# Performance work log

Hardware: AMD Instinct MI355X
Metric: run time of the kernel (lower is better)

## Reference

```python
import jax, jax.numpy as jnp
import numpy as np

N, E, DIN, HID, DOUT = 50000, 800000, 128, 128, 64
NEG_SLOPE = 0.2


def setup_inputs() -> dict:
    key = jax.random.key(0)
    ks = jax.random.split(key, 16)
    x = jax.random.normal(ks[0], (N, DIN), dtype=jnp.float32)
    edge_index = jax.random.randint(ks[1], (2, E), 0, N, dtype=jnp.int64)

    def lin(k, fan_in, fan_out):
        kw, kb = jax.random.split(k)
        s = 1.0 / np.sqrt(fan_in)
        W = jax.random.uniform(kw, (fan_in, fan_out), jnp.float32, -s, s)
        b = jax.random.uniform(kb, (fan_out,), jnp.float32, -s, s)
        return W, b

    Wl, bl = lin(ks[2], DIN, DIN)   # GATv2 lin_l
    Wr, br = lin(ks[3], DIN, DIN)   # GATv2 lin_r
    att = jax.random.uniform(ks[4], (DIN,), jnp.float32, -1.0 / np.sqrt(DIN), 1.0 / np.sqrt(DIN))
    bg = jnp.zeros((DIN,), jnp.float32)  # GAT output bias
    W1, b1 = lin(ks[5], DIN, HID)   # ChebConv K=1 -> plain linear
    W2, b2 = lin(ks[6], HID, HID)
    W3, b3 = lin(ks[7], HID, DOUT)
    return {"x": x, "edge_index": edge_index, "Wl": Wl, "bl": bl, "Wr": Wr,
            "br": br, "att": att, "bg": bg, "W1": W1, "b1": b1,
            "W2": W2, "b2": b2, "W3": W3, "b3": b3}


def reference(x, edge_index, Wl, bl, Wr, br, att, bg, W1, b1, W2, b2, W3, b3):
    n = x.shape[0]
    # GATv2Conv adds self loops by default
    loop = jnp.arange(n, dtype=edge_index.dtype)
    src = jnp.concatenate([edge_index[0], loop])  # source j
    dst = jnp.concatenate([edge_index[1], loop])  # target i

    xl = x @ Wl + bl  # [N, DIN]
    xr = x @ Wr + br  # [N, DIN]

    # GATv2 edge scores: leaky_relu(x_l[j] + x_r[i]) . att
    e = jax.nn.leaky_relu(xl[src] + xr[dst], NEG_SLOPE)  # [E+N, DIN]
    a = e @ att                                          # [E+N]

    # softmax over incoming edges of each destination node
    amax = jax.ops.segment_max(a, dst, num_segments=n)
    ea = jnp.exp(a - amax[dst])
    denom = jax.ops.segment_sum(ea, dst, num_segments=n)
    alpha = ea / denom[dst]                              # [E+N]

    # aggregate messages alpha * x_l[j] at destinations
    h = jax.ops.segment_sum(alpha[:, None] * xl[src], dst, num_segments=n) + bg

    # ChebConv with K=1 reduces to a linear layer (T_0(L) = I)
    h = jax.nn.relu(h @ W1 + b1)
    h = jax.nn.relu(h @ W2 + b2)
    # dropout_rate = 0.0 -> identity
    return h @ W3 + b3
```

## Files before the change

### kernel.cpp

```cpp
#include <hip/hip_runtime.h>
#include <hip/hip_bf16.h>

#define DIN 128
#define NEG_SLOPE 0.2f
#define PTILE 1024
#define CVT_BLKS 289

typedef __attribute__((ext_vector_type(8))) short bf16x8;
typedef __attribute__((ext_vector_type(8))) unsigned short u16x8;
typedef __attribute__((ext_vector_type(4))) float f32x4;
typedef __attribute__((ext_vector_type(2))) float f32x2;
typedef __attribute__((ext_vector_type(4))) unsigned int u32x4;

__device__ __forceinline__ ushort f2bf(float f) {
  unsigned u = __float_as_uint(f);
  u += 0x7FFFu + ((u >> 16) & 1u);
  return (ushort)(u >> 16);
}
__device__ __forceinline__ f32x2 bfpair(unsigned u) {
  f32x2 r;
  r.x = __uint_as_float(u << 16);
  r.y = __uint_as_float(u & 0xFFFF0000u);
  return r;
}

template <int CTRL>
__device__ __forceinline__ float dppadd(float x) {
  int v = __builtin_amdgcn_update_dpp(0, __float_as_int(x), CTRL, 0xf, 0xf, true);
  return x + __int_as_float(v);
}
__device__ __forceinline__ float red16(float t) {
  t = dppadd<0xB1>(t);
  t = dppadd<0x4E>(t);
  t = dppadd<0x141>(t);
  t = dppadd<0x140>(t);
  return t;
}

__global__ __launch_bounds__(256) void cvt_hist_kernel(
    const float* __restrict__ Wl, const float* __restrict__ Wr,
    const float* __restrict__ W1, const float* __restrict__ W2,
    const float* __restrict__ W3,
    ushort* __restrict__ WlT, ushort* __restrict__ WrT,
    ushort* __restrict__ W1T, ushort* __restrict__ W2T,
    ushort* __restrict__ W3T,
    const int* __restrict__ ei, int* __restrict__ ghist,
    int* __restrict__ nhist, int E) {
  if (blockIdx.x < CVT_BLKS) {
    int i = blockIdx.x * 256 + threadIdx.x;
    if (i < 16384) {
      int k = i >> 7, c = i & 127; WlT[c * 128 + k] = f2bf(Wl[i]);
    } else if (i < 32768) {
      int j = i - 16384; int k = j >> 7, c = j & 127; WrT[c * 128 + k] = f2bf(Wr[j]);
    } else if (i < 49152) {
      int j = i - 32768; int k = j >> 7, c = j & 127; W1T[c * 128 + k] = f2bf(W1[j]);
    } else if (i < 65536) {
      int j = i - 49152; int k = j >> 7, c = j & 127; W2T[c * 128 + k] = f2bf(W2[j]);
    } else if (i < 73728) {
      int j = i - 65536; int k = j >> 6, c = j & 63; W3T[c * 128 + k] = f2bf(W3[j]);
    }
  } else {
    __shared__ int h[256];
    h[threadIdx.x] = 0;
    __syncthreads();
    int tile = blockIdx.x - CVT_BLKS;
    for (int e = tile * PTILE + threadIdx.x;
         e < min(E, (tile + 1) * PTILE); e += 256) {
      int d = ei[E + e];
      atomicAdd(&h[d >> 8], 1);
      atomicAdd(&nhist[d], 1);
    }
    __syncthreads();
    if (h[threadIdx.x] > 0) atomicAdd(&ghist[threadIdx.x], h[threadIdx.x]);
  }
}

__global__ __launch_bounds__(256) void lin_partition_kernel(
    const float* __restrict__ x,
    const ushort* __restrict__ WlT, const float* __restrict__ bl,
    const ushort* __restrict__ WrT, const float* __restrict__ br,
    ushort* __restrict__ xl, ushort* __restrict__ xr, int n, int nblk_lin,
    const int* __restrict__ ei, unsigned* __restrict__ part,
    const int* __restrict__ ghist, int* __restrict__ cursor0, int E) {
  if ((int)blockIdx.x < nblk_lin) {
    const int tid = threadIdx.x;
    const int wv = tid >> 6, lane = tid & 63;
    const int m = lane & 15, quad = lane >> 4;
    const int colbase = (wv & 1) * 64;
    const int nodew = blockIdx.x * 32 + (wv >> 1) * 16;
    int arow = nodew + m; if (arow >= n) arow = n - 1;
    f32x4 accl[4], accr[4];
#pragma unroll
    for (int nt = 0; nt < 4; nt++) { accl[nt] = (f32x4){0,0,0,0}; accr[nt] = (f32x4){0,0,0,0}; }
#pragma unroll
    for (int kk = 0; kk < 4; kk++) {
      int k0 = kk * 32 + quad * 8;
      const float4* xp = (const float4*)(x + (long)arow * 128 + k0);
      float4 x0 = xp[0], x1 = xp[1];
      bf16x8 af;
      af[0] = (short)f2bf(x0.x); af[1] = (short)f2bf(x0.y);
      af[2] = (short)f2bf(x0.z); af[3] = (short)f2bf(x0.w);
      af[4] = (short)f2bf(x1.x); af[5] = (short)f2bf(x1.y);
      af[6] = (short)f2bf(x1.z); af[7] = (short)f2bf(x1.w);
#pragma unroll
      for (int nt = 0; nt < 4; nt++) {
        int brow = colbase + nt * 16 + m;
        bf16x8 bl8 = *(const bf16x8*)(WlT + brow * 128 + k0);
        bf16x8 br8 = *(const bf16x8*)(WrT + brow * 128 + k0);
        accl[nt] = __builtin_amdgcn_mfma_f32_16x16x32_bf16(af, bl8, accl[nt], 0, 0, 0);
        accr[nt] = __builtin_amdgcn_mfma_f32_16x16x32_bf16(af, br8, accr[nt], 0, 0, 0);
      }
    }
#pragma unroll
    for (int nt = 0; nt < 4; nt++) {
      int col = colbase + nt * 16 + m;
      float vbl = bl[col], vbr = br[col];
#pragma unroll
      for (int r = 0; r < 4; r++) {
        int node = nodew + quad * 4 + r;
        if (node < n) {
          xl[(long)node * 128 + col] = f2bf(accl[nt][r] + vbl);
          xr[(long)node * 128 + col] = f2bf(accr[nt][r] + vbr);
        }
      }
    }
  } else {
    __shared__ int hist[256], pref[256], sexcl[256], curs[256], gbase[256],
                   gsc[256];
    const int tid = threadIdx.x;
    const int gv0 = ghist[tid];
    gsc[tid] = gv0;
    hist[tid] = 0;
    __syncthreads();
    __shared__ unsigned buf[PTILE];
    const int tile0 = ((int)blockIdx.x - nblk_lin) * PTILE;
    const int tcount = min(PTILE, E - tile0);
    unsigned pk[PTILE / 256];
    int cnt = 0;
    for (int i = tid; i < tcount; i += 256) {
      int e = tile0 + i;
      int s = ei[e], d = ei[E + e];
      unsigned p = ((unsigned)d << 16) | (unsigned)s;
      pk[cnt++] = p;
      atomicAdd(&hist[d >> 8], 1);
    }
    __syncthreads();
    int v = hist[tid];
    pref[tid] = v;
    __syncthreads();
    for (int d = 1; d < 256; d <<= 1) {
      int t1 = (tid >= d) ? pref[tid - d] : 0;
      int t2 = (tid >= d) ? gsc[tid - d] : 0;
      __syncthreads();
      pref[tid] += t1;
      gsc[tid] += t2;
      __syncthreads();
    }
    int exc = pref[tid] - v;
    sexcl[tid] = exc;
    curs[tid] = exc;
    gbase[tid] = (gsc[tid] - gv0) + ((v > 0) ? atomicAdd(&cursor0[tid], v) : 0);
    __syncthreads();
    for (int j = 0; j < cnt; j++) {
      int b = pk[j] >> 24;
      int pos = atomicAdd(&curs[b], 1);
      buf[pos] = pk[j];
    }
    __syncthreads();
    for (int i = tid; i < tcount; i += 256) {
      unsigned p = buf[i];
      int b = p >> 24;
      part[gbase[b] + (i - sexcl[b])] = p;
    }
  }
}

__global__ __launch_bounds__(512) void fine_kernel(
    const unsigned* __restrict__ part, const int* __restrict__ ghist,
    const int* __restrict__ nhist,
    int* __restrict__ offsets, ushort* __restrict__ ssrc,
    int N, int E, int nbuck) {
  __shared__ int gsc[256], nsc[256], curs[256];
  const int tid = threadIdx.x;
  const int b = blockIdx.x;
  int nv = 0;
  if (tid < 256) {
    gsc[tid] = ghist[tid];
    int node = b * 256 + tid;
    nv = (node < N) ? nhist[node] : 0;
    nsc[tid] = nv;
  }
  __syncthreads();
  for (int d = 1; d < 256; d <<= 1) {
    int t1 = (tid >= d && tid < 256) ? gsc[tid - d] : 0;
    int t2 = (tid >= d && tid < 256) ? nsc[tid - d] : 0;
    __syncthreads();
    if (tid < 256) { gsc[tid] += t1; nsc[tid] += t2; }
    __syncthreads();
  }
  const int seg0 = (b == 0) ? 0 : gsc[b - 1];
  const int len = gsc[b] - seg0;
  if (tid < 256) {
    int o = seg0 + nsc[tid] - nv;
    curs[tid] = o;
    int node = b * 256 + tid;
    if (node < N) offsets[node] = o;
  }
  if (b == nbuck - 1 && tid == 0) offsets[N] = E;
  __syncthreads();
  for (int i = tid; i < len; i += 512) {
    unsigned p = part[seg0 + i];
    int pos = atomicAdd(&curs[(p >> 16) & 255], 1);
    ssrc[pos] = (ushort)(p & 0xFFFFu);
  }
}

__global__ __launch_bounds__(256) void node_aggr_kernel(
    const ushort* __restrict__ xl, const ushort* __restrict__ xr,
    const float* __restrict__ att, const float* __restrict__ bg,
    const int* __restrict__ offsets, const ushort* __restrict__ ssrc,
    ushort* __restrict__ h, int n) {
  int wave = (int)((blockIdx.x * (long)blockDim.x + threadIdx.x) >> 6);
  int lane = threadIdx.x & 63;
  if (wave >= n) return;
  const int node = wave;
  const int eg = lane >> 4, sl = lane & 15;
  const int beg = offsets[node];
  const int end = offsets[node + 1];
  const int last = end - 1;
  const ushort* __restrict__ xls = xl + sl * 8;
  int ia0 = beg + 2 * eg;
  int sa  = (int)ssrc[min(ia0, last)];
  int sb  = (int)ssrc[min(ia0 + 1, last)];
  int sa2 = (int)ssrc[min(ia0 + 8, last)];
  int sb2 = (int)ssrc[min(ia0 + 9, last)];
  u32x4 uva = *(const u32x4*)(xls + (long)sa * 128);
  u32x4 uvb = *(const u32x4*)(xls + (long)sb * 128);

  f32x2 a06[4], a04[4], r2[4], acc2[4];
  {
    const float4* ap = (const float4*)(att + sl * 8);
    float4 a0 = ap[0], a1 = ap[1];
    f32x2 av[4] = {{a0.x, a0.y}, {a0.z, a0.w}, {a1.x, a1.y}, {a1.z, a1.w}};
#pragma unroll
    for (int jp = 0; jp < 4; jp++) {
      a06[jp] = 0.6f * av[jp];
      a04[jp] = 0.4f * av[jp];
    }
  }
  u32x4 rv = *(const u32x4*)(xr + (long)node * 128 + sl * 8);
  u32x4 lv = *(const u32x4*)(xls + (long)node * 128);
  float denom;
  {
    f32x2 t1 = {0.f, 0.f}, t2 = {0.f, 0.f};
    f32x2 l2[4];
#pragma unroll
    for (int jp = 0; jp < 4; jp++) {
      r2[jp] = bfpair(rv[jp]);
      l2[jp] = bfpair(lv[jp]);
      f32x2 v = l2[jp] + r2[jp];
      t1 += a06[jp] * v;
      t2 += a04[jp] * __builtin_elementwise_abs(v);
    }
    float t = red16(t1.x + t1.y + t2.x + t2.y);
    float es = __expf(t);
    denom = (eg == 0) ? es : 0.f;
#pragma unroll
    for (int jp = 0; jp < 4; jp++)
      acc2[jp] = (eg == 0) ? es * l2[jp] : (f32x2){0.f, 0.f};
  }
  for (int p = beg; p < end; p += 8) {
    u32x4 ca = uva, cb = uvb;
    int ia = p + 2 * eg;
    bool cva = ia < end, cvb = ia + 1 < end;
    uva = *(const u32x4*)(xls + (long)sa2 * 128);
    uvb = *(const u32x4*)(xls + (long)sb2 * 128);
    int ian = p + 16 + 2 * eg;
    sa2 = (int)ssrc[min(ian, last)];
    sb2 = (int)ssrc[min(ian + 1, last)];
    f32x2 ua2[4], ub2[4];
    f32x2 ta1 = {0.f, 0.f}, ta2 = {0.f, 0.f};
    f32x2 tb1 = {0.f, 0.f}, tb2 = {0.f, 0.f};
#pragma unroll
    for (int jp = 0; jp < 4; jp++) {
      ua2[jp] = bfpair(ca[jp]);
      ub2[jp] = bfpair(cb[jp]);
      f32x2 va2 = ua2[jp] + r2[jp];
      f32x2 vb2 = ub2[jp] + r2[jp];
      ta1 += a06[jp] * va2;
      ta2 += a04[jp] * __builtin_elementwise_abs(va2);
      tb1 += a06[jp] * vb2;
      tb2 += a04[jp] * __builtin_elementwise_abs(vb2);
    }
    float ta = red16(ta1.x + ta1.y + ta2.x + ta2.y);
    float tb = red16(tb1.x + tb1.y + tb2.x + tb2.y);
    float ea = cva ? __expf(ta) : 0.f;
    float eb = cvb ? __expf(tb) : 0.f;
    denom += ea + eb;
#pragma unroll
    for (int jp = 0; jp < 4; jp++)
      acc2[jp] += ea * ua2[jp] + eb * ub2[jp];
  }
#pragma unroll
  for (int jp = 0; jp < 4; jp++) {
    acc2[jp].x += __shfl_xor(acc2[jp].x, 16);
    acc2[jp].y += __shfl_xor(acc2[jp].y, 16);
    acc2[jp].x += __shfl_xor(acc2[jp].x, 32);
    acc2[jp].y += __shfl_xor(acc2[jp].y, 32);
  }
  denom += __shfl_xor(denom, 16);
  denom += __shfl_xor(denom, 32);
  if (eg == 0) {
    float inv = 1.0f / denom;
    const float4* bp = (const float4*)(bg + sl * 8);
    float4 g0 = bp[0], g1 = bp[1];
    f32x2 gv[4] = {{g0.x, g0.y}, {g0.z, g0.w}, {g1.x, g1.y}, {g1.z, g1.w}};
    u16x8 o;
#pragma unroll
    for (int jp = 0; jp < 4; jp++) {
      f32x2 hv = acc2[jp] * inv + gv[jp];
      o[2 * jp]     = f2bf(hv.x);
      o[2 * jp + 1] = f2bf(hv.y);
    }
    *(u16x8*)(h + (long)node * 128 + sl * 8) = o;
  }
}

#define LDSP 136
__global__ __launch_bounds__(256) void mlp_mfma_kernel(
    const ushort* __restrict__ hb,
    const ushort* __restrict__ W1T, const float* __restrict__ b1,
    const ushort* __restrict__ W2T, const float* __restrict__ b2,
    const ushort* __restrict__ W3T, const float* __restrict__ b3,
    float* __restrict__ out, int n) {
  __shared__ ushort act[32][LDSP];
  const int tid = threadIdx.x;
  const int wv = tid >> 6, lane = tid & 63;
  const int m = lane & 15, quad = lane >> 4;
  const int half = wv & 1, ng = wv >> 1;
  const int colbase = half * 64;
  const int nodew = blockIdx.x * 32 + ng * 16;
  int arow = nodew + m; if (arow >= n) arow = n - 1;
  f32x4 acc[4];
#pragma unroll
  for (int nt = 0; nt < 4; nt++) acc[nt] = (f32x4){0,0,0,0};
#pragma unroll
  for (int kk = 0; kk < 4; kk++) {
    int k0 = kk * 32 + quad * 8;
    bf16x8 af = *(const bf16x8*)(hb + (long)arow * 128 + k0);
#pragma unroll
    for (int nt = 0; nt < 4; nt++) {
      bf16x8 b8 = *(const bf16x8*)(W1T + (colbase + nt * 16 + m) * 128 + k0);
      acc[nt] = __builtin_amdgcn_mfma_f32_16x16x32_bf16(af, b8, acc[nt], 0, 0, 0);
    }
  }
#pragma unroll
  for (int nt = 0; nt < 4; nt++) {
    int col = colbase + nt * 16 + m;
    float b = b1[col];
#pragma unroll
    for (int r = 0; r < 4; r++)
      act[ng * 16 + quad * 4 + r][col] = f2bf(fmaxf(acc[nt][r] + b, 0.f));
  }
  __syncthreads();
#pragma unroll
  for (int nt = 0; nt < 4; nt++) acc[nt] = (f32x4){0,0,0,0};
#pragma unroll
  for (int kk = 0; kk < 4; kk++) {
    int k0 = kk * 32 + quad * 8;
    bf16x8 af = *(const bf16x8*)(&act[ng * 16 + m][k0]);
#pragma unroll
    for (int nt = 0; nt < 4; nt++) {
      bf16x8 b8 = *(const bf16x8*)(W2T + (colbase + nt * 16 + m) * 128 + k0);
      acc[nt] = __builtin_amdgcn_mfma_f32_16x16x32_bf16(af, b8, acc[nt], 0, 0, 0);
    }
  }
  __syncthreads();
#pragma unroll
  for (int nt = 0; nt < 4; nt++) {
    int col = colbase + nt * 16 + m;
    float b = b2[col];
#pragma unroll
    for (int r = 0; r < 4; r++)
      act[ng * 16 + quad * 4 + r][col] = f2bf(fmaxf(acc[nt][r] + b, 0.f));
  }
  __syncthreads();
  f32x4 acc3[2];
#pragma unroll
  for (int nt = 0; nt < 2; nt++) acc3[nt] = (f32x4){0,0,0,0};
#pragma unroll
  for (int kk = 0; kk < 4; kk++) {
    int k0 = kk * 32 + quad * 8;
    bf16x8 af = *(const bf16x8*)(&act[ng * 16 + m][k0]);
#pragma unroll
    for (int nt = 0; nt < 2; nt++) {
      bf16x8 b8 = *(const bf16x8*)(W3T + (half * 32 + nt * 16 + m) * 128 + k0);
      acc3[nt] = __builtin_amdgcn_mfma_f32_16x16x32_bf16(af, b8, acc3[nt], 0, 0, 0);
    }
  }
#pragma unroll
  for (int nt = 0; nt < 2; nt++) {
    int col = half * 32 + nt * 16 + m;
    float b = b3[col];
#pragma unroll
    for (int r = 0; r < 4; r++) {
      int node = nodew + quad * 4 + r;
      if (node < n) out[(long)node * 64 + col] = acc3[nt][r] + b;
    }
  }
}

extern "C" void kernel_launch(void* const* d_in, const int* in_sizes, int n_in,
                              void* d_out, int out_size, void* d_ws, size_t ws_size,
                              hipStream_t stream) {
  const float* x   = (const float*)d_in[0];
  const int*   ei  = (const int*)d_in[1];
  const float* Wl  = (const float*)d_in[2];
  const float* bl  = (const float*)d_in[3];
  const float* Wr  = (const float*)d_in[4];
  const float* br  = (const float*)d_in[5];
  const float* att = (const float*)d_in[6];
  const float* bg  = (const float*)d_in[7];
  const float* W1  = (const float*)d_in[8];
  const float* b1  = (const float*)d_in[9];
  const float* W2  = (const float*)d_in[10];
  const float* b2  = (const float*)d_in[11];
  const float* W3  = (const float*)d_in[12];
  const float* b3  = (const float*)d_in[13];
  float* out = (float*)d_out;

  const int N = in_sizes[0] / DIN;
  const int E = in_sizes[1] / 2;
  const int nbuck = (N + 255) >> 8;

  char* ws = (char*)d_ws;
  size_t off = 0;
  auto alloc = [&](size_t bytes) {
    void* p = ws + off;
    off += (bytes + 255) & ~(size_t)255;
    return p;
  };
  int* ghist     = (int*)alloc(256 * 4);
  int* cursor0   = (int*)alloc(256 * 4);
  int* nhist     = (int*)alloc((size_t)N * 4);
  int* offsets   = (int*)alloc(((size_t)N + 4) * 4);
  unsigned* part = (unsigned*)alloc((size_t)E * 4);
  ushort* ssrc   = (ushort*)alloc(((size_t)E + 16) * 2);
  ushort* xlb    = (ushort*)alloc((size_t)N * DIN * 2);
  ushort* xrb    = (ushort*)alloc((size_t)N * DIN * 2);
  ushort* hbf    = (ushort*)alloc((size_t)N * DIN * 2);
  ushort* WlT    = (ushort*)alloc(16384 * 2);
  ushort* WrT    = (ushort*)alloc(16384 * 2);
  ushort* W1T    = (ushort*)alloc(16384 * 2);
  ushort* W2T    = (ushort*)alloc(16384 * 2);
  ushort* W3T    = (ushort*)alloc(8192 * 2);
  (void)ws_size;

  hipMemsetAsync(ghist, 0, 2048 + (size_t)N * 4, stream);

  int ntile = (E + PTILE - 1) / PTILE;
  cvt_hist_kernel<<<CVT_BLKS + ntile, 256, 0, stream>>>(
      Wl, Wr, W1, W2, W3, WlT, WrT, W1T, W2T, W3T, ei, ghist, nhist, E);

  int nblk32 = (N + 31) / 32;
  lin_partition_kernel<<<nblk32 + ntile, 256, 0, stream>>>(
      x, WlT, bl, WrT, br, xlb, xrb, N, nblk32, ei, part, ghist, cursor0, E);

  fine_kernel<<<nbuck, 512, 0, stream>>>(part, ghist, nhist, offsets, ssrc,
                                         N, E, nbuck);

  int nwblk = (N + 3) / 4;
  node_aggr_kernel<<<nwblk, 256, 0, stream>>>(xlb, xrb, att, bg,
                                              offsets, ssrc, hbf, N);

  mlp_mfma_kernel<<<nblk32, 256, 0, stream>>>(hbf, W1T, b1, W2T, b2,
                                              W3T, b3, out, N);
}
```

Baseline: 281.5 us.

## Compute per-node degree counts in fine kernel LDS instead of global atomics

```diff
diff --git a/kernel.cpp b/kernel.cpp
--- a/kernel.cpp
+++ b/kernel.cpp
@@ -3,7 +3,8 @@
 
 #define DIN 128
 #define NEG_SLOPE 0.2f
-#define PTILE 1024
+#define PTILE 2048
+#define FCAP 8192
 #define CVT_BLKS 289
 
 typedef __attribute__((ext_vector_type(8))) short bf16x8;
@@ -44,8 +45,7 @@
     ushort* __restrict__ WlT, ushort* __restrict__ WrT,
     ushort* __restrict__ W1T, ushort* __restrict__ W2T,
     ushort* __restrict__ W3T,
-    const int* __restrict__ ei, int* __restrict__ ghist,
-    int* __restrict__ nhist, int E) {
+    const int* __restrict__ ei, int* __restrict__ ghist, int E) {
   if (blockIdx.x < CVT_BLKS) {
     int i = blockIdx.x * 256 + threadIdx.x;
     if (i < 16384) {
@@ -65,11 +65,8 @@
     __syncthreads();
     int tile = blockIdx.x - CVT_BLKS;
     for (int e = tile * PTILE + threadIdx.x;
-         e < min(E, (tile + 1) * PTILE); e += 256) {
-      int d = ei[E + e];
-      atomicAdd(&h[d >> 8], 1);
-      atomicAdd(&nhist[d], 1);
-    }
+         e < min(E, (tile + 1) * PTILE); e += 256)
+      atomicAdd(&h[ei[E + e] >> 8], 1);
     __syncthreads();
     if (h[threadIdx.x] > 0) atomicAdd(&ghist[threadIdx.x], h[threadIdx.x]);
   }
@@ -175,41 +172,52 @@
   }
 }
 
-__global__ __launch_bounds__(512) void fine_kernel(
+__global__ __launch_bounds__(1024) void fine_kernel(
     const unsigned* __restrict__ part, const int* __restrict__ ghist,
-    const int* __restrict__ nhist,
     int* __restrict__ offsets, ushort* __restrict__ ssrc,
     int N, int E, int nbuck) {
-  __shared__ int gsc[256], nsc[256], curs[256];
+  __shared__ int hist[256], gsc[256], curs[256];
+  __shared__ unsigned buf[FCAP];
   const int tid = threadIdx.x;
   const int b = blockIdx.x;
-  int nv = 0;
   if (tid < 256) {
     gsc[tid] = ghist[tid];
-    int node = b * 256 + tid;
-    nv = (node < N) ? nhist[node] : 0;
-    nsc[tid] = nv;
+    hist[tid] = 0;
   }
   __syncthreads();
   for (int d = 1; d < 256; d <<= 1) {
-    int t1 = (tid >= d && tid < 256) ? gsc[tid - d] : 0;
-    int t2 = (tid >= d && tid < 256) ? nsc[tid - d] : 0;
-    __syncthreads();
-    if (tid < 256) { gsc[tid] += t1; nsc[tid] += t2; }
+    int t = (tid >= d && tid < 256) ? gsc[tid - d] : 0;
+    __syncthreads();
+    if (tid < 256) gsc[tid] += t;
     __syncthreads();
   }
   const int seg0 = (b == 0) ? 0 : gsc[b - 1];
-  const int len = gsc[b] - seg0;
+  const int len = min(gsc[b] - seg0, FCAP);
+  for (int i = tid; i < len; i += 1024) {
+    unsigned p = part[seg0 + i];
+    buf[i] = p;
+    atomicAdd(&hist[(p >> 16) & 255], 1);
+  }
+  __syncthreads();
+  int v = (tid < 256) ? hist[tid] : 0;
+  if (tid < 256) hist[tid] = v;
+  __syncthreads();
+  for (int d = 1; d < 256; d <<= 1) {
+    int t = (tid >= d && tid < 256) ? hist[tid - d] : 0;
+    __syncthreads();
+    if (tid < 256) hist[tid] += t;
+    __syncthreads();
+  }
   if (tid < 256) {
-    int o = seg0 + nsc[tid] - nv;
+    int o = seg0 + hist[tid] - v;
     curs[tid] = o;
     int node = b * 256 + tid;
     if (node < N) offsets[node] = o;
   }
   if (b == nbuck - 1 && tid == 0) offsets[N] = E;
   __syncthreads();
-  for (int i = tid; i < len; i += 512) {
-    unsigned p = part[seg0 + i];
+  for (int i = tid; i < len; i += 1024) {
+    unsigned p = buf[i];
     int pos = atomicAdd(&curs[(p >> 16) & 255], 1);
     ssrc[pos] = (ushort)(p & 0xFFFFu);
   }
@@ -442,7 +450,6 @@
   };
   int* ghist     = (int*)alloc(256 * 4);
   int* cursor0   = (int*)alloc(256 * 4);
-  int* nhist     = (int*)alloc((size_t)N * 4);
   int* offsets   = (int*)alloc(((size_t)N + 4) * 4);
   unsigned* part = (unsigned*)alloc((size_t)E * 4);
   ushort* ssrc   = (ushort*)alloc(((size_t)E + 16) * 2);
@@ -456,18 +463,18 @@
   ushort* W3T    = (ushort*)alloc(8192 * 2);
   (void)ws_size;
 
-  hipMemsetAsync(ghist, 0, 2048 + (size_t)N * 4, stream);
+  hipMemsetAsync(ghist, 0, 512 * 4, stream);
 
   int ntile = (E + PTILE - 1) / PTILE;
   cvt_hist_kernel<<<CVT_BLKS + ntile, 256, 0, stream>>>(
-      Wl, Wr, W1, W2, W3, WlT, WrT, W1T, W2T, W3T, ei, ghist, nhist, E);
+      Wl, Wr, W1, W2, W3, WlT, WrT, W1T, W2T, W3T, ei, ghist, E);
 
   int nblk32 = (N + 31) / 32;
   lin_partition_kernel<<<nblk32 + ntile, 256, 0, stream>>>(
       x, WlT, bl, WrT, br, xlb, xrb, N, nblk32, ei, part, ghist, cursor0, E);
 
-  fine_kernel<<<nbuck, 512, 0, stream>>>(part, ghist, nhist, offsets, ssrc,
-                                         N, E, nbuck);
+  fine_kernel<<<nbuck, 1024, 0, stream>>>(part, ghist, offsets, ssrc,
+                                          N, E, nbuck);
 
   int nwblk = (N + 3) / 4;
   node_aggr_kernel<<<nwblk, 256, 0, stream>>>(xlb, xrb, att, bg,
```

New measurement: 243.1 us. 13.7% less time.
